# Optimization experiments

Measured on AMD Instinct MI355X. Metric: run time of the kernel, lower is better.

Reference implementation:

```python
import jax, jax.numpy as jnp
import numpy as np

F = 65536          # num_face
W_DIM = 512
PAD = 4096         # zero pad rows appended before gather
LRELU_SLOPE = 0.2
LRELU_GAIN = np.sqrt(2.0).astype(np.float32)  # def_gain of lrelu


def _fc(w, W, b):
    # StyleGAN FullyConnectedLayer: x @ W.T / sqrt(in_features) + bias
    gain = np.float32(1.0 / np.sqrt(W.shape[1]))
    return w @ W.T * gain + b


def _faceconv_gather(x, neigh, is_pad, k):
    # x: [B*F, C]; neigh/is_pad: [B*F, 9]; take first k neighbor slots.
    padded = jnp.concatenate([x, jnp.zeros((PAD, x.shape[1]), x.dtype)], axis=0)
    g = padded[neigh[:, :k]]                      # [B*F, k, C] irregular gather
    return jnp.where(is_pad[:, :k, None], jnp.zeros((), x.dtype), g)


def _modulated_face_conv(g, weight, styles, demodulate):
    # g: [B*F, k, I]; weight: [O, I, 1, k]; styles: [B, I]
    B = styles.shape[0]
    w = weight[None, :, :, 0, :] * styles[:, None, :, None]      # [B, O, I, k]
    if demodulate:
        d = jax.lax.rsqrt(jnp.sum(w * w, axis=(2, 3)) + 1e-8)    # [B, O]
        w = w * d[:, :, None, None]
    gb = g.reshape(B, -1, g.shape[1], g.shape[2])                # [B, F, k, I]
    out = jnp.einsum('bfki,boik->bfo', gb, w)                    # [B, F, O]
    return out.reshape(-1, w.shape[1])


def setup_inputs() -> dict:
    key = jax.random.key(0)
    ks = jax.random.split(key, 12)
    B = 2
    C = 128
    N = B * F
    face_neighborhood = jax.random.randint(ks[0], (N, 9), 0, N + PAD, dtype=jnp.int64)
    face_is_pad = jax.random.randint(ks[1], (N, 9), 0, 10) == 0
    return {
        'face_neighborhood': face_neighborhood,
        'face_is_pad': face_is_pad,
        'ws': jax.random.normal(ks[2], (B, 2, W_DIM), jnp.float32),
        'const': jax.random.normal(ks[3], (F, C), jnp.float32),
        'affine1_W': jax.random.normal(ks[4], (C, W_DIM), jnp.float32),
        'affine1_b': jnp.ones((C,), jnp.float32),
        'weight1': jax.random.normal(ks[5], (C, C, 1, 9), jnp.float32),
        'noise_const': jax.random.normal(ks[6], (F,), jnp.float32),
        'noise_strength': jnp.zeros((1,), jnp.float32),
        'bias1': jnp.zeros((C,), jnp.float32),
        'affine2_W': jax.random.normal(ks[7], (C, W_DIM), jnp.float32),
        'affine2_b': jnp.ones((C,), jnp.float32),
        'weight2': jax.random.normal(ks[8], (3, C, 1, 1), jnp.float32),
        'bias2': jnp.zeros((3,), jnp.float32),
    }


def reference(face_neighborhood, face_is_pad, ws, const, affine1_W, affine1_b,
              weight1, noise_const, noise_strength, bias1, affine2_W, affine2_b,
              weight2, bias2):
    # noise_mode == 'const'
    B = ws.shape[0]
    w0, w1 = ws[:, 0], ws[:, 1]
    x = jnp.tile(const[None], (B, 1, 1)).reshape(B * F, -1)        # [B*F, C]

    # --- SynthesisLayer conv1 ---
    styles = _fc(w0, affine1_W, affine1_b)                         # [B, C]
    noise = jnp.tile(noise_const[None], (B, 1)).reshape(-1, 1) * noise_strength
    g = _faceconv_gather(x, face_neighborhood, face_is_pad, 9)     # [B*F, 9, C]
    x = _modulated_face_conv(g, weight1, styles, demodulate=True)  # [B*F, C]
    x = x + noise
    x = jax.nn.leaky_relu(x + bias1[None, :], LRELU_SLOPE)
    x = jnp.clip(x * LRELU_GAIN, -256.0, 256.0)                    # clamp_gain

    # --- ToRGBLayer ---
    wg = np.float32(1.0 / np.sqrt(weight2.shape[1] * 1))
    styles2 = _fc(w1, affine2_W, affine2_b) * wg
    g2 = _faceconv_gather(x, face_neighborhood, face_is_pad, 1)    # [B*F, 1, C]
    img = _modulated_face_conv(g2, weight2, styles2, demodulate=False)
    img = jnp.clip(img + bias2[None, :], -256.0, 256.0)
    return x, img
```

## Files before the change

### kernel.cpp

```cpp
#include <hip/hip_runtime.h>

typedef unsigned short u16;
typedef __bf16 bf16x8 __attribute__((ext_vector_type(8)));
typedef float f32x4 __attribute__((ext_vector_type(4)));
typedef unsigned short u16x8 __attribute__((ext_vector_type(8)));

#define F_FACES 65536
#define N_FACES 131072
#define C_CH 128
#define WS_W2F 256
#define WS_W1 5376
#define WS_CONST 595200
#define XELEMS 16777216

__device__ inline u16 f2bf(float f) {
    unsigned u = __builtin_bit_cast(unsigned, f);
    unsigned r = (u + 0x7fffu + ((u >> 16) & 1u)) >> 16;
    return (u16)r;
}

__device__ inline void gl_lds16(const void* g, void* l) {
    __builtin_amdgcn_global_load_lds(
        (const __attribute__((address_space(1))) void*)g,
        (__attribute__((address_space(3))) void*)l, 16, 0, 0);
}

__device__ inline f32x4 nt_load4(const float* p) {
    return __builtin_nontemporal_load((const f32x4*)p);
}

__global__ __launch_bounds__(256) void k0_all(
    const float* __restrict__ wsv, const float* __restrict__ a1W, const float* __restrict__ a1b,
    const float* __restrict__ a2W, const float* __restrict__ a2b,
    const float* __restrict__ cst, const float* __restrict__ w1g,
    const float* __restrict__ w2, unsigned char* __restrict__ wsb)
{
    __shared__ float part[2][128];
    __shared__ float s1sh[128];
    __shared__ float red[4];
    int bid = blockIdx.x;
    int tid = threadIdx.x;

    if (bid >= 257) {
        u16* dst = (u16*)(wsb + WS_CONST);
        int base = ((bid - 257) * 256 + tid) * 8;
        f32x4 a = nt_load4(cst + base);
        f32x4 c = nt_load4(cst + base + 4);
        u16x8 p;
        p[0] = f2bf(a[0]); p[1] = f2bf(a[1]); p[2] = f2bf(a[2]); p[3] = f2bf(a[3]);
        p[4] = f2bf(c[0]); p[5] = f2bf(c[1]); p[6] = f2bf(c[2]); p[7] = f2bf(c[3]);
        *(u16x8*)(dst + base) = p;
        return;
    }
    const float g512 = 0.04419417382415922f;
    const float g128 = 0.08838834764831845f;
    if (bid < 256) {
        int b = bid >> 7, o = bid & 127;
        int h = tid >> 7, i = tid & 127;
        {
            const float4* xr = (const float4*)(wsv + (size_t)(b * 2 + 0) * 512) + h * 64;
            const float4* ar = (const float4*)(a1W + (size_t)i * 512) + h * 64;
            float p = 0.f;
#pragma unroll 8
            for (int j = 0; j < 64; ++j) {
                float4 w4 = ar[j], x4 = xr[j];
                p += w4.x * x4.x + w4.y * x4.y + w4.z * x4.z + w4.w * x4.w;
            }
            part[h][i] = p;
        }
        __syncthreads();
        if (tid < 128) s1sh[tid] = (part[0][tid] + part[1][tid]) * g512 + a1b[tid];
        __syncthreads();
        float sum = 0.f;
        for (int e = tid; e < 1152; e += 256) {
            int ii = e / 9;
            float w = w1g[(size_t)o * 1152 + e] * s1sh[ii];
            sum += w * w;
        }
        int wv = tid >> 6, lane = tid & 63;
#pragma unroll
        for (int d = 1; d < 64; d <<= 1) sum += __shfl_xor(sum, d);
        if (lane == 0) red[wv] = sum;
        __syncthreads();
        float dm = rsqrtf(red[0] + red[1] + red[2] + red[3] + 1e-8f);
        u16* w1out = (u16*)(wsb + WS_W1);
        for (int wd = tid; wd < 576; wd += 256) {
            int k = wd >> 6;
            int ii = (wd & 63) * 2;
            float v0 = w1g[((size_t)o * 128 + ii) * 9 + k] * s1sh[ii] * dm;
            float v1 = w1g[((size_t)o * 128 + ii + 1) * 9 + k] * s1sh[ii + 1] * dm;
            unsigned pack = (unsigned)f2bf(v0) | ((unsigned)f2bf(v1) << 16);
            *(unsigned*)&w1out[(size_t)((((b * 9 + k) * 16 + (ii >> 3)) * 128 + o) * 8 + (ii & 7))] = pack;
        }
        return;
    }
    {
        float* s2sh = &part[0][0];
        int b = tid >> 7, i = tid & 127;
        const float4* xr = (const float4*)(wsv + (size_t)(b * 2 + 1) * 512);
        const float4* ar = (const float4*)(a2W + (size_t)i * 512);
        float p = 0.f;
#pragma unroll 8
        for (int j = 0; j < 128; ++j) {
            float4 w4 = ar[j], x4 = xr[j];
            p += w4.x * x4.x + w4.y * x4.y + w4.z * x4.z + w4.w * x4.w;
        }
        s2sh[tid] = (p * g512 + a2b[i]) * g128;
        __syncthreads();
        float* wsf = (float*)wsb;
        if (tid < 64) wsf[tid] = 0.f;
#pragma unroll
        for (int r = 0; r < 3; ++r) {
            int id = tid + r * 256;
            int b2 = id / 384;
            int rem = id - b2 * 384;
            int o2 = rem >> 7;
            int ii = rem & 127;
            wsf[WS_W2F / 4 + id] = w2[o2 * 128 + ii] * s2sh[b2 * 128 + ii];
        }
    }
}

__global__ __launch_bounds__(256, 5) void k1_conv(
    const int* __restrict__ neigh, const int* __restrict__ ispad,
    const float* __restrict__ noise_c, const float* __restrict__ nstr,
    const float* __restrict__ bias1, const unsigned char* __restrict__ wsb,
    float* __restrict__ out)
{
    __shared__ __align__(16) u16 As[2][64 * 128];

    const int tid = threadIdx.x;
    const int wv = tid >> 6, lane = tid & 63;
    const int quad = lane >> 4, l15 = lane & 15;
    const int f0 = blockIdx.x * 64;
    const int b = f0 >> 16;
    const u16* cst = (const u16*)(wsb + WS_CONST);
    const u16* w1ws = (const u16*)(wsb + WS_W1) + (size_t)b * 147456;
    const char* zp = (const char*)wsb;

    f32x4 acc[4][2] = {};
    int ia[4], ip[4];

#pragma unroll
    for (int r = 0; r < 4; ++r) {
        int nb = (f0 + (wv * 4 + r) * 4 + quad) * 9 + 0;
        ia[r] = neigh[nb]; ip[r] = ispad[nb];
    }
#pragma unroll
    for (int r = 0; r < 4; ++r) {
        int row = (wv * 4 + r) * 4 + quad;
        bool valid = (ip[r] == 0) && ((unsigned)ia[r] < 131072u);
        const char* src = valid ? (const char*)(cst + ((size_t)(ia[r] & 65535) << 7)) : zp;
        gl_lds16(src + ((l15 ^ (row & 15)) << 4), (char*)(&As[0][0]) + ((wv * 4 + r) << 10));
    }
#pragma unroll
    for (int r = 0; r < 4; ++r) {
        int nb = (f0 + (wv * 4 + r) * 4 + quad) * 9 + 1;
        ia[r] = neigh[nb]; ip[r] = ispad[nb];
    }

#pragma unroll
    for (int k = 0; k < 9; ++k) {
        bf16x8 bfr[4][2];
#pragma unroll
        for (int s = 0; s < 4; ++s)
#pragma unroll
            for (int nt = 0; nt < 2; ++nt)
                bfr[s][nt] = *reinterpret_cast<const bf16x8*>(
                    w1ws + (((k * 16 + s * 4 + quad) * 128) + wv * 32 + nt * 16 + l15) * 8);
        asm volatile("" ::: "memory");
        __builtin_amdgcn_sched_barrier(0);

        if (k < 8) {
#pragma unroll
            for (int r = 0; r < 4; ++r) {
                int row = (wv * 4 + r) * 4 + quad;
                bool valid = (ip[r] == 0) && ((unsigned)ia[r] < 131072u);
                const char* src = valid ? (const char*)(cst + ((size_t)(ia[r] & 65535) << 7)) : zp;
                gl_lds16(src + ((l15 ^ (row & 15)) << 4),
                         (char*)(&As[(k + 1) & 1][0]) + ((wv * 4 + r) << 10));
            }
        }
        if (k < 7) {
#pragma unroll
            for (int r = 0; r < 4; ++r) {
                int nb = (f0 + (wv * 4 + r) * 4 + quad) * 9 + (k + 2);
                ia[r] = neigh[nb]; ip[r] = ispad[nb];
            }
        }
        if (k < 7)       asm volatile("s_waitcnt vmcnt(20)" ::: "memory");
        else if (k == 7) asm volatile("s_waitcnt vmcnt(12)" ::: "memory");
        else             asm volatile("s_waitcnt vmcnt(8)" ::: "memory");
        __builtin_amdgcn_s_barrier();
        __builtin_amdgcn_sched_barrier(0);

        const u16* Ab = &As[k & 1][0];
#pragma unroll
        for (int s = 0; s < 4; ++s) {
            bf16x8 af[4];
#pragma unroll
            for (int mt = 0; mt < 4; ++mt) {
                int face = mt * 16 + l15;
                int chunk = (s * 4 + quad) ^ l15;
                af[mt] = *reinterpret_cast<const bf16x8*>(&Ab[face * 128 + chunk * 8]);
            }
#pragma unroll
            for (int mt = 0; mt < 4; ++mt)
#pragma unroll
                for (int nt = 0; nt < 2; ++nt)
                    acc[mt][nt] = __builtin_amdgcn_mfma_f32_16x16x32_bf16(
                        af[mt], bfr[s][nt], acc[mt][nt], 0, 0, 0);
        }
        asm volatile("s_waitcnt lgkmcnt(0)" ::: "memory");
        __builtin_amdgcn_s_barrier();
        __builtin_amdgcn_sched_barrier(0);
    }

    float ns = nstr[0];
    float b1v[2];
    b1v[0] = bias1[wv * 32 + l15];
    b1v[1] = bias1[wv * 32 + 16 + l15];
#pragma unroll
    for (int mt = 0; mt < 4; ++mt) {
#pragma unroll
        for (int r = 0; r < 4; ++r) {
            int face = f0 + mt * 16 + quad * 4 + r;
            float nz = noise_c[face & 65535] * ns;
#pragma unroll
            for (int nt = 0; nt < 2; ++nt) {
                float v = acc[mt][nt][r] + nz + b1v[nt];
                v = (v > 0.f) ? v : 0.2f * v;
                v *= 1.41421356f;
                v = fminf(fmaxf(v, -256.f), 256.f);
                __builtin_nontemporal_store(v, &out[(size_t)face * 128 + wv * 32 + nt * 16 + l15]);
            }
        }
    }
}

__global__ __launch_bounds__(256) void k2_img(
    const int* __restrict__ neigh, const int* __restrict__ ispad,
    const float* __restrict__ w2f, const float* __restrict__ bias2,
    const float* __restrict__ xbuf, float* __restrict__ imgout)
{
    int tid = threadIdx.x;
    int wv = tid >> 6, lane = tid & 63;
    int g = lane >> 4, sub = lane & 15;
    int face = blockIdx.x * 16 + wv * 4 + g;
    int b = face >> 16;
    int idx = neigh[face * 9];
    bool valid = (ispad[face * 9] == 0) && ((unsigned)idx < 131072u);
    float a0 = 0.f, a1 = 0.f, a2 = 0.f;
    if (valid) {
        const float* xr = xbuf + (size_t)idx * 128 + sub * 8;
        f32x4 d0 = nt_load4(xr);
        f32x4 d1 = nt_load4(xr + 4);
        const float4* w04 = (const float4*)(w2f + (b * 3 + 0) * 128 + sub * 8);
        const float4* w14 = (const float4*)(w2f + (b * 3 + 1) * 128 + sub * 8);
        const float4* w24 = (const float4*)(w2f + (b * 3 + 2) * 128 + sub * 8);
        float4 w0a = w04[0], w0b = w04[1];
        float4 w1a = w14[0], w1b = w14[1];
        float4 w2a = w24[0], w2b = w24[1];
        a0 = d0[0] * w0a.x + d0[1] * w0a.y + d0[2] * w0a.z + d0[3] * w0a.w
           + d1[0] * w0b.x + d1[1] * w0b.y + d1[2] * w0b.z + d1[3] * w0b.w;
        a1 = d0[0] * w1a.x + d0[1] * w1a.y + d0[2] * w1a.z + d0[3] * w1a.w
           + d1[0] * w1b.x + d1[1] * w1b.y + d1[2] * w1b.z + d1[3] * w1b.w;
        a2 = d0[0] * w2a.x + d0[1] * w2a.y + d0[2] * w2a.z + d0[3] * w2a.w
           + d1[0] * w2b.x + d1[1] * w2b.y + d1[2] * w2b.z + d1[3] * w2b.w;
    }
#pragma unroll
    for (int d = 1; d < 16; d <<= 1) {
        a0 += __shfl_xor(a0, d);
        a1 += __shfl_xor(a1, d);
        a2 += __shfl_xor(a2, d);
    }
    if (sub < 3) {
        float v = (sub == 0) ? a0 : (sub == 1) ? a1 : a2;
        v += bias2[sub];
        v = fminf(fmaxf(v, -256.f), 256.f);
        __builtin_nontemporal_store(v, &imgout[face * 3 + sub]);
    }
}

extern "C" void kernel_launch(void* const* d_in, const int* in_sizes, int n_in,
                              void* d_out, int out_size, void* d_ws, size_t ws_size,
                              hipStream_t stream) {
    const int* neigh = (const int*)d_in[0];
    const int* ispad = (const int*)d_in[1];
    const float* wsv = (const float*)d_in[2];
    const float* cst = (const float*)d_in[3];
    const float* a1W = (const float*)d_in[4];
    const float* a1b = (const float*)d_in[5];
    const float* w1g = (const float*)d_in[6];
    const float* noise_c = (const float*)d_in[7];
    const float* nstr = (const float*)d_in[8];
    const float* bias1 = (const float*)d_in[9];
    const float* a2W = (const float*)d_in[10];
    const float* a2b = (const float*)d_in[11];
    const float* w2 = (const float*)d_in[12];
    const float* bias2 = (const float*)d_in[13];
    float* out = (float*)d_out;
    unsigned char* wsb = (unsigned char*)d_ws;

    k0_all<<<4353, 256, 0, stream>>>(wsv, a1W, a1b, a2W, a2b, cst, w1g, w2, wsb);
    k1_conv<<<2048, 256, 0, stream>>>(neigh, ispad, noise_c, nstr, bias1, wsb, out);
    k2_img<<<8192, 256, 0, stream>>>(neigh, ispad, (const float*)(wsb + WS_W2F), bias2,
                                     out, out + XELEMS);
}
```

Before: 228.4 us.

## Precompute per-face ToRGB projections in conv epilogue, gather small table in img kernel

The conv1 epilogue now projects each output row onto the 3x128 ToRGB weights for both styles, reduces the partial sums across lanes and waves through LDS, and writes a 6-float-per-face table. The image kernel then gathers 3 floats per face instead of a 512-byte row of x, and runs one thread per face. This moves the second gather's bandwidth into a small table, at the price of extra shuffles, an LDS reduction and a block barrier in conv1. The output stores also switch from nontemporal to normal stores.

After: 240.8 us. +5.5%, slower.

```diff
diff --git a/kernel.cpp b/kernel.cpp
--- a/kernel.cpp
+++ b/kernel.cpp
@@ -11,6 +11,7 @@
 #define WS_W2F 256
 #define WS_W1 5376
 #define WS_CONST 595200
+#define WS_Y 17372416
 #define XELEMS 16777216
 
 __device__ inline u16 f2bf(float f) {
@@ -125,7 +126,7 @@
     const int* __restrict__ neigh, const int* __restrict__ ispad,
     const float* __restrict__ noise_c, const float* __restrict__ nstr,
     const float* __restrict__ bias1, const unsigned char* __restrict__ wsb,
-    float* __restrict__ out)
+    float* __restrict__ out, float* __restrict__ ytab)
 {
     __shared__ __align__(16) u16 As[2][64 * 128];
 
@@ -220,66 +221,72 @@
     float b1v[2];
     b1v[0] = bias1[wv * 32 + l15];
     b1v[1] = bias1[wv * 32 + 16 + l15];
+    const float* w2f = (const float*)(wsb + WS_W2F);
+    float w2v[2][3][2];
+#pragma unroll
+    for (int b2 = 0; b2 < 2; ++b2)
+#pragma unroll
+        for (int o = 0; o < 3; ++o)
+#pragma unroll
+            for (int nt = 0; nt < 2; ++nt)
+                w2v[b2][o][nt] = w2f[(b2 * 3 + o) * 128 + wv * 32 + nt * 16 + l15];
+
+    float* red = (float*)&As[0][0];
 #pragma unroll
     for (int mt = 0; mt < 4; ++mt) {
 #pragma unroll
         for (int r = 0; r < 4; ++r) {
-            int face = f0 + mt * 16 + quad * 4 + r;
+            int fl = mt * 16 + quad * 4 + r;
+            int face = f0 + fl;
             float nz = noise_c[face & 65535] * ns;
+            float vv[2];
 #pragma unroll
             for (int nt = 0; nt < 2; ++nt) {
                 float v = acc[mt][nt][r] + nz + b1v[nt];
                 v = (v > 0.f) ? v : 0.2f * v;
                 v *= 1.41421356f;
                 v = fminf(fmaxf(v, -256.f), 256.f);
-                __builtin_nontemporal_store(v, &out[(size_t)face * 128 + wv * 32 + nt * 16 + l15]);
-            }
-        }
+                out[(size_t)face * 128 + wv * 32 + nt * 16 + l15] = v;
+                vv[nt] = v;
+            }
+#pragma unroll
+            for (int j = 0; j < 6; ++j) {
+                float pp = vv[0] * w2v[j / 3][j % 3][0] + vv[1] * w2v[j / 3][j % 3][1];
+#pragma unroll
+                for (int d = 1; d < 16; d <<= 1) pp += __shfl_xor(pp, d);
+                if (l15 == 0) red[fl * 24 + wv * 6 + j] = pp;
+            }
+        }
+    }
+    __syncthreads();
+    for (int t = tid; t < 384; t += 256) {
+        int fl = t / 6, j = t - fl * 6;
+        float y = red[fl * 24 + j] + red[fl * 24 + 6 + j]
+                + red[fl * 24 + 12 + j] + red[fl * 24 + 18 + j];
+        ytab[(size_t)(f0 + fl) * 6 + j] = y;
     }
 }
 
 __global__ __launch_bounds__(256) void k2_img(
     const int* __restrict__ neigh, const int* __restrict__ ispad,
-    const float* __restrict__ w2f, const float* __restrict__ bias2,
-    const float* __restrict__ xbuf, float* __restrict__ imgout)
+    const float* __restrict__ ytab, const float* __restrict__ bias2,
+    float* __restrict__ imgout)
 {
-    int tid = threadIdx.x;
-    int wv = tid >> 6, lane = tid & 63;
-    int g = lane >> 4, sub = lane & 15;
-    int face = blockIdx.x * 16 + wv * 4 + g;
-    int b = face >> 16;
-    int idx = neigh[face * 9];
-    bool valid = (ispad[face * 9] == 0) && ((unsigned)idx < 131072u);
-    float a0 = 0.f, a1 = 0.f, a2 = 0.f;
+    int f = blockIdx.x * 256 + threadIdx.x;
+    int b = f >> 16;
+    int idx = neigh[(size_t)f * 9];
+    bool valid = (ispad[(size_t)f * 9] == 0) && ((unsigned)idx < 131072u);
+    float v0 = 0.f, v1 = 0.f, v2 = 0.f;
     if (valid) {
-        const float* xr = xbuf + (size_t)idx * 128 + sub * 8;
-        f32x4 d0 = nt_load4(xr);
-        f32x4 d1 = nt_load4(xr + 4);
-        const float4* w04 = (const float4*)(w2f + (b * 3 + 0) * 128 + sub * 8);
-        const float4* w14 = (const float4*)(w2f + (b * 3 + 1) * 128 + sub * 8);
-        const float4* w24 = (const float4*)(w2f + (b * 3 + 2) * 128 + sub * 8);
-        float4 w0a = w04[0], w0b = w04[1];
-        float4 w1a = w14[0], w1b = w14[1];
-        float4 w2a = w24[0], w2b = w24[1];
-        a0 = d0[0] * w0a.x + d0[1] * w0a.y + d0[2] * w0a.z + d0[3] * w0a.w
-           + d1[0] * w0b.x + d1[1] * w0b.y + d1[2] * w0b.z + d1[3] * w0b.w;
-        a1 = d0[0] * w1a.x + d0[1] * w1a.y + d0[2] * w1a.z + d0[3] * w1a.w
-           + d1[0] * w1b.x + d1[1] * w1b.y + d1[2] * w1b.z + d1[3] * w1b.w;
-        a2 = d0[0] * w2a.x + d0[1] * w2a.y + d0[2] * w2a.z + d0[3] * w2a.w
-           + d1[0] * w2b.x + d1[1] * w2b.y + d1[2] * w2b.z + d1[3] * w2b.w;
-    }
-#pragma unroll
-    for (int d = 1; d < 16; d <<= 1) {
-        a0 += __shfl_xor(a0, d);
-        a1 += __shfl_xor(a1, d);
-        a2 += __shfl_xor(a2, d);
-    }
-    if (sub < 3) {
-        float v = (sub == 0) ? a0 : (sub == 1) ? a1 : a2;
-        v += bias2[sub];
-        v = fminf(fmaxf(v, -256.f), 256.f);
-        __builtin_nontemporal_store(v, &imgout[face * 3 + sub]);
-    }
+        const float* y = ytab + (size_t)idx * 6 + b * 3;
+        v0 = y[0]; v1 = y[1]; v2 = y[2];
+    }
+    v0 = fminf(fmaxf(v0 + bias2[0], -256.f), 256.f);
+    v1 = fminf(fmaxf(v1 + bias2[1], -256.f), 256.f);
+    v2 = fminf(fmaxf(v2 + bias2[2], -256.f), 256.f);
+    imgout[(size_t)f * 3 + 0] = v0;
+    imgout[(size_t)f * 3 + 1] = v1;
+    imgout[(size_t)f * 3 + 2] = v2;
 }
 
 extern "C" void kernel_launch(void* const* d_in, const int* in_sizes, int n_in,
@@ -301,9 +308,9 @@
     const float* bias2 = (const float*)d_in[13];
     float* out = (float*)d_out;
     unsigned char* wsb = (unsigned char*)d_ws;
+    float* ytab = (float*)(wsb + WS_Y);
 
     k0_all<<<4353, 256, 0, stream>>>(wsv, a1W, a1b, a2W, a2b, cst, w1g, w2, wsb);
-    k1_conv<<<2048, 256, 0, stream>>>(neigh, ispad, noise_c, nstr, bias1, wsb, out);
-    k2_img<<<8192, 256, 0, stream>>>(neigh, ispad, (const float*)(wsb + WS_W2F), bias2,
-                                     out, out + XELEMS);
-}
+    k1_conv<<<2048, 256, 0, stream>>>(neigh, ispad, noise_c, nstr, bias1, wsb, out, ytab);
+    k2_img<<<512, 256, 0, stream>>>(neigh, ispad, ytab, bias2, out + XELEMS);
+}
```
